# Kernel tuning notes

Hardware: AMD Instinct MI355X
Metric: run time of the kernel (lower is better)

## Reference

```python
import jax, jax.numpy as jnp
import numpy as np

BATCH, T, HID = 4, 2048, 1024
H = P = 1024  # input_dim and ssm_size (expand_ratio=1.0)
EPS = 1e-5
DISCRETIZATION = "IM"  # 'IM' or 'IMEX'


def setup_inputs() -> dict:
    key = jax.random.key(0)
    ks = jax.random.split(key, 10)
    std_b = 1.0 / np.sqrt(H)
    std_c = 1.0 / np.sqrt(P)
    u = lambda k, s, lo, hi: jax.random.uniform(k, s, jnp.float32, lo, hi)
    return {
        "hidden_states": jax.random.normal(ks[0], (BATCH, T, HID), jnp.float32),
        "Wi": jax.random.normal(ks[1], (H, HID), jnp.float32) / np.sqrt(HID),
        "Wg": jax.random.normal(ks[2], (H, HID), jnp.float32) / np.sqrt(HID),
        "Wo": jax.random.normal(ks[3], (HID, H), jnp.float32) / np.sqrt(H),
        "A_diag": u(ks[4], (P,), 0.0, 1.0),
        "B_param": u(ks[5], (P, H, 2), -std_b, std_b),
        "C_param": u(ks[6], (H, P, 2), -std_c, std_c),
        "D": jax.random.normal(ks[7], (H,), jnp.float32),
        "dt": u(ks[8], (P,), 0.0, 1.0),
        "norm_weight": jnp.ones((H,), jnp.float32),
    }


def _linoss(x, B_param, C_param, A_diag, dt_p, D):
    """LinOSS oscillatory SSM recurrence with complex B/C and diagonal A.
    x: (B,T,H) real input. State z,y in C^P (re/im stacked on last axis)."""
    A = jax.nn.relu(A_diag)       # (P,) nonneg frequencies
    dt = jax.nn.sigmoid(dt_p)     # (P,) timesteps in (0,1)
    # Bu_{re,im}[b,t,p] = sum_h x[b,t,h] * B_{re,im}[p,h]
    Bu = jnp.einsum('bth,phc->btpc', x, B_param)  # (B,T,P,2)
    if DISCRETIZATION == "IM":
        S = 1.0 / (1.0 + dt * dt * A)
        m11, m12, m21, m22 = S, -dt * A * S, dt * S, S
        f1, f2 = dt * S, dt * dt * S
    else:  # IMEX
        one = jnp.ones_like(dt)
        m11, m12, m21, m22 = one, -dt * A, dt, 1.0 - dt * dt * A
        f1, f2 = dt, dt * dt
    c = lambda v: v[None, :, None]  # broadcast (P,) -> (B,P,2)

    def step(carry, bu):
        z, y = carry  # each (B,P,2)
        z1 = c(m11) * z + c(m12) * y + c(f1) * bu
        y1 = c(m21) * z + c(m22) * y + c(f2) * bu
        return (z1, y1), y1

    z0 = jnp.zeros((x.shape[0], A.shape[0], 2), x.dtype)
    _, ys = jax.lax.scan(step, (z0, z0), jnp.swapaxes(Bu, 0, 1))
    ys = jnp.swapaxes(ys, 0, 1)  # (B,T,P,2)
    # o = Re(C @ y) + D * x
    o = (jnp.einsum('btp,hp->bth', ys[..., 0], C_param[..., 0])
         - jnp.einsum('btp,hp->bth', ys[..., 1], C_param[..., 1]))
    return o + x * D


def reference(hidden_states, Wi, Wg, Wo, A_diag, B_param, C_param, D, dt, norm_weight):
    x = hidden_states @ Wi.T                        # i_proj
    o = _linoss(x, B_param, C_param, A_diag, dt, D)  # fused_recurrent_linoss
    g = hidden_states @ Wg.T                        # g_proj
    # FusedRMSNormGated: rmsnorm(o) * weight * swish(g)
    o = o * jax.lax.rsqrt(jnp.mean(o * o, axis=-1, keepdims=True) + EPS) * norm_weight
    o = o * (g * jax.nn.sigmoid(g))
    return o @ Wo.T                                  # o_proj
```

## Files before the change

kernel.cpp:

```cpp
#include <hip/hip_runtime.h>
#include <hip/hip_bf16.h>
#include <math.h>

#define BB 4
#define TT 2048
#define HH 1024
#define PP 1024
#define MT 8192
#define C2 2048
#define NC 64
#define LCH 32

typedef __attribute__((ext_vector_type(8))) short  bf16x8;
typedef __attribute__((ext_vector_type(4))) float  f32x4;

__device__ __forceinline__ ushort f2bf(float f) {
    union { float f; unsigned u; } v; v.f = f;
    unsigned r = v.u + 0x7fffu + ((v.u >> 16) & 1u);
    return (ushort)(r >> 16);
}
__device__ __forceinline__ float bf2f(ushort h) {
    union { unsigned u; float f; } v; v.u = ((unsigned)h) << 16;
    return v.f;
}

__device__ __forceinline__ void gload16(const ushort* g, ushort* l) {
    __builtin_amdgcn_global_load_lds((const __attribute__((address_space(1))) void*)g,
                                     (__attribute__((address_space(3))) void*)l,
                                     16, 0, 0);
}
__device__ __forceinline__ void barrier_raw() { __builtin_amdgcn_s_barrier(); }
__device__ __forceinline__ void lgk0() { asm volatile("s_waitcnt lgkmcnt(0)" ::: "memory"); }
__device__ __forceinline__ void vm6()  { asm volatile("s_waitcnt vmcnt(6)"   ::: "memory"); }
__device__ __forceinline__ void vm0()  { asm volatile("s_waitcnt vmcnt(0)"   ::: "memory"); }

__global__ void convert_all(const float* __restrict__ hs, const float* __restrict__ Wi,
                            const float* __restrict__ Wg, const float* __restrict__ Wo,
                            ushort* __restrict__ hsb, ushort* __restrict__ Wigb,
                            ushort* __restrict__ Wob) {
    int i = blockIdx.x * 256 + threadIdx.x;
    const int HS4 = MT * HH / 4;
    const int W4  = HH * HH / 4;
    const float4* s;
    ushort4* d;
    if (i < HS4)               { s = (const float4*)hs + i;               d = (ushort4*)hsb  + i; }
    else if (i < HS4 + 2 * W4) { int j = i - HS4;
                                 s = (const float4*)(j < W4 ? Wi : Wg) + (j < W4 ? j : j - W4);
                                 d = (ushort4*)Wigb + j; }
    else                       { int j = i - HS4 - 2 * W4;
                                 s = (const float4*)Wo + j;               d = (ushort4*)Wob + j; }
    float4 v = *s;
    ushort4 o;
    o.x = f2bf(v.x); o.y = f2bf(v.y); o.z = f2bf(v.z); o.w = f2bf(v.w);
    *d = o;
}

__global__ void repack_B_bf(const float* __restrict__ src, ushort* __restrict__ dst) {
    int idx = blockIdx.x * 256 + threadIdx.x;
    int p = idx >> 10;
    int h = idx & 1023;
    float2 v = ((const float2*)src)[idx];
    dst[(size_t)p * HH + h]        = f2bf(v.x);
    dst[(size_t)(p + PP) * HH + h] = f2bf(v.y);
}

__global__ void repack_C_bf(const float* __restrict__ src, ushort* __restrict__ dst) {
    int idx = blockIdx.x * 256 + threadIdx.x;
    int h = idx >> 10;
    int p = idx & 1023;
    float2 v = ((const float2*)src)[idx];
    dst[(size_t)h * C2 + p]      = f2bf(v.x);
    dst[(size_t)h * C2 + PP + p] = f2bf(-v.y);
}

template<int BM, int STORE_BF16>
__global__ __launch_bounds__(512, 2) void gemm8p(
    const ushort* __restrict__ A, int lda,
    const ushort* __restrict__ B, int ldb,
    void* __restrict__ Cp, int ldc, int K, int nbx)
{
    constexpr int BN  = 256;
    constexpr int MR  = BM / 32;
    constexpr int MRH = MR / 2;
    constexpr int TA  = BM * 128;
    constexpr int TB  = BN * 128;
    __shared__ __align__(16) char smem[2 * TA + 2 * TB];

    const int bid = blockIdx.x;
    const int cpx = gridDim.x >> 3;
    const int wg  = (bid & 7) * cpx + (bid >> 3);
    const int by  = wg / nbx;
    const int bx  = wg - by * nbx;
    const int bm  = by * BM;
    const int bn  = bx * BN;

    const int tid  = threadIdx.x;
    const int wave = tid >> 6;
    const int lane = tid & 63;
    const int wr   = wave >> 2;
    const int wc   = wave & 3;
    const int lr   = lane & 15;
    const int kg   = lane >> 4;

    const int e  = (wave << 10) + ((lane << 4) ^ (((lane >> 3) & 7) << 4));
    const int r0 = e >> 7;
    const int c0 = (e & 127) >> 1;

    auto stA = [&](int bi, int u, int kt) {
        gload16(A + (size_t)(bm + u * 64 + r0) * lda + kt * 64 + c0,
                (ushort*)(smem + bi * TA + u * 8192 + (wave << 10)));
    };
    auto stB = [&](int bi, int u, int kt) {
        gload16(B + (size_t)(bn + u * 64 + r0) * ldb + kt * 64 + c0,
                (ushort*)(smem + 2 * TA + bi * TB + u * 8192 + (wave << 10)));
    };

    bf16x8 Af[MRH][2], Bf[4][2];
    auto ldsA = [&](int bi, int qm) {
#pragma unroll
        for (int f = 0; f < MRH; ++f)
#pragma unroll
            for (int kk = 0; kk < 2; ++kk) {
                int row = wr * (BM / 2) + qm * (BM / 4) + f * 16 + lr;
                int o = row * 128 + kk * 64 + kg * 16;
                o ^= (row & 7) << 4;
                Af[f][kk] = *(const bf16x8*)(smem + bi * TA + o);
            }
    };
    auto ldsB = [&](int bi) {
#pragma unroll
        for (int n = 0; n < 4; ++n)
#pragma unroll
            for (int kk = 0; kk < 2; ++kk) {
                int row = wc * 64 + n * 16 + lr;
                int o = row * 128 + kk * 64 + kg * 16;
                o ^= (row & 7) << 4;
                Bf[n][kk] = *(const bf16x8*)(smem + 2 * TA + bi * TB + o);
            }
    };

    f32x4 acc[MR][4];
#pragma unroll
    for (int m = 0; m < MR; ++m)
#pragma unroll
        for (int n = 0; n < 4; ++n)
#pragma unroll
            for (int i = 0; i < 4; ++i) acc[m][n][i] = 0.f;

    auto mfma16 = [&](int qm, int qn) {
        __builtin_amdgcn_s_setprio(1);
#pragma unroll
        for (int f = 0; f < MRH; ++f)
#pragma unroll
            for (int n2 = 0; n2 < 2; ++n2)
#pragma unroll
                for (int kk = 0; kk < 2; ++kk)
                    acc[qm * MRH + f][qn * 2 + n2] =
                        __builtin_amdgcn_mfma_f32_16x16x32_bf16(
                            Af[f][kk], Bf[qn * 2 + n2][kk],
                            acc[qm * MRH + f][qn * 2 + n2], 0, 0, 0);
        __builtin_amdgcn_s_setprio(0);
    };

    if constexpr (BM == 256) {
        stA(0, 0, 0); stA(0, 1, 0); stA(0, 2, 0); stA(0, 3, 0);
        stB(0, 0, 0); stB(0, 1, 0); stB(0, 2, 0); stB(0, 3, 0);
        stB(1, 0, 1); stB(1, 1, 1); stB(1, 2, 1); stB(1, 3, 1);
        stA(1, 0, 1); stA(1, 2, 1);
    } else {
        stA(0, 0, 0); stA(0, 1, 0);
        stB(0, 0, 0); stB(0, 1, 0); stB(0, 2, 0); stB(0, 3, 0);
        stA(1, 0, 1); stA(1, 1, 1);
        stB(1, 0, 1); stB(1, 1, 1); stB(1, 2, 1); stB(1, 3, 1);
    }
    vm6();
    barrier_raw();

    const int nIter = K >> 7;
    for (int J = 0; J < nIter; ++J) {
        const bool pf  = (J + 1 < nIter);
        const int  kt1 = 2 * J + 1, kt2 = 2 * J + 2, kt3 = 2 * J + 3;
        ldsA(0, 0); ldsB(0);
        if constexpr (BM == 256) { stA(1, 1, kt1); stA(1, 3, kt1); }
        barrier_raw(); lgk0(); mfma16(0, 0); barrier_raw();
        if (pf) { stB(0, 0, kt2); stB(0, 1, kt2); }
        barrier_raw(); lgk0(); mfma16(0, 1); barrier_raw();
        ldsA(0, 1);
        if (pf) { stB(0, 2, kt2); stB(0, 3, kt2); }
        barrier_raw(); lgk0(); mfma16(1, 0); barrier_raw();
        if (pf) {
            if constexpr (BM == 256) { stA(0, 0, kt2); stA(0, 2, kt2); }
            else                     { stA(0, 0, kt2); stA(0, 1, kt2); }
        }
        barrier_raw(); lgk0(); mfma16(1, 1);
        if (pf) vm6(); else vm0();
        barrier_raw();
        ldsA(1, 0); ldsB(1);
        if constexpr (BM == 256) { if (pf) { stA(0, 1, kt2); stA(0, 3, kt2); } }
        barrier_raw(); lgk0(); mfma16(0, 0); barrier_raw();
        if (pf) { stB(1, 0, kt3); stB(1, 1, kt3); }
        barrier_raw(); lgk0(); mfma16(0, 1); barrier_raw();
        ldsA(1, 1);
        if (pf) { stB(1, 2, kt3); stB(1, 3, kt3); }
        barrier_raw(); lgk0(); mfma16(1, 0); barrier_raw();
        if (pf) {
            if constexpr (BM == 256) { stA(1, 0, kt3); stA(1, 2, kt3); }
            else                     { stA(1, 0, kt3); stA(1, 1, kt3); }
        }
        barrier_raw(); lgk0(); mfma16(1, 1);
        if (pf) vm6(); else vm0();
        barrier_raw();
    }

#pragma unroll
    for (int mf = 0; mf < MR; ++mf) {
#pragma unroll
        for (int n = 0; n < 4; ++n) {
            int col = bn + wc * 64 + n * 16 + lr;
#pragma unroll
            for (int i = 0; i < 4; ++i) {
                int row = bm + wr * (BM / 2) + mf * 16 + kg * 4 + i;
                float v = acc[mf][n][i];
                if (STORE_BF16)
                    ((ushort*)Cp)[(size_t)row * ldc + col] = f2bf(v);
                else
                    ((float*)Cp)[(size_t)row * ldc + col]  = v;
            }
        }
    }
}

__device__ __forceinline__ void linoss_coeffs(const float* A_diag, const float* dt_p,
                                              int p, float& m11, float& m12,
                                              float& m21, float& m22,
                                              float& f1, float& f2) {
    float A  = fmaxf(A_diag[p], 0.f);
    float dt = 1.f / (1.f + expf(-dt_p[p]));
    float S  = 1.f / (1.f + dt * dt * A);
    m11 = S;        m12 = -dt * A * S;
    m21 = dt * S;   m22 = S;
    f1  = dt * S;   f2  = dt * dt * S;
}

__global__ void scan_passA(const ushort* __restrict__ Bu,
                           const float* __restrict__ A_diag,
                           const float* __restrict__ dt_p,
                           float2* __restrict__ sEnd) {
    int c = blockIdx.x * 256 + threadIdx.x;
    int b = blockIdx.y;
    int j = blockIdx.z;
    float m11, m12, m21, m22, f1, f2;
    linoss_coeffs(A_diag, dt_p, c & 1023, m11, m12, m21, m22, f1, f2);
    const ushort* bu = Bu + ((size_t)(b * TT + j * LCH)) * C2 + c;
    float z = 0.f, y = 0.f;
#pragma unroll 8
    for (int i = 0; i < LCH; ++i) {
        float u  = bf2f(bu[(size_t)i * C2]);
        float z1 = m11 * z + m12 * y + f1 * u;
        float y1 = m21 * z + m22 * y + f2 * u;
        z = z1; y = y1;
    }
    sEnd[((size_t)j * BB + b) * C2 + c] = make_float2(z, y);
}

__global__ void scan_combine(const float* __restrict__ A_diag,
                             const float* __restrict__ dt_p,
                             const float2* __restrict__ sEnd,
                             float2* __restrict__ sInit) {
    int idx = blockIdx.x * 256 + threadIdx.x;
    int c = idx & (C2 - 1);
    int b = idx >> 11;
    float m11, m12, m21, m22, f1, f2;
    linoss_coeffs(A_diag, dt_p, c & 1023, m11, m12, m21, m22, f1, f2);
    float e11 = m11, e12 = m12, e21 = m21, e22 = m22;
#pragma unroll
    for (int s = 0; s < 5; ++s) {
        float n11 = e11 * e11 + e12 * e21;
        float n12 = e11 * e12 + e12 * e22;
        float n21 = e21 * e11 + e22 * e21;
        float n22 = e21 * e12 + e22 * e22;
        e11 = n11; e12 = n12; e21 = n21; e22 = n22;
    }
    float z = 0.f, y = 0.f;
    for (int j = 0; j < NC; ++j) {
        size_t off = ((size_t)j * BB + b) * C2 + c;
        sInit[off] = make_float2(z, y);
        float2 le = sEnd[off];
        float z1 = e11 * z + e12 * y + le.x;
        float y1 = e21 * z + e22 * y + le.y;
        z = z1; y = y1;
    }
}

__global__ void scan_passB(const ushort* __restrict__ Bu,
                           const float* __restrict__ A_diag,
                           const float* __restrict__ dt_p,
                           const float2* __restrict__ sInit,
                           ushort* __restrict__ YSb) {
    int c = blockIdx.x * 256 + threadIdx.x;
    int b = blockIdx.y;
    int j = blockIdx.z;
    float m11, m12, m21, m22, f1, f2;
    linoss_coeffs(A_diag, dt_p, c & 1023, m11, m12, m21, m22, f1, f2);
    float2 s0 = sInit[((size_t)j * BB + b) * C2 + c];
    float z = s0.x, y = s0.y;
    const ushort* bu = Bu  + ((size_t)(b * TT + j * LCH)) * C2 + c;
    ushort*       ys = YSb + ((size_t)(b * TT + j * LCH)) * C2 + c;
#pragma unroll 8
    for (int i = 0; i < LCH; ++i) {
        float u  = bf2f(bu[(size_t)i * C2]);
        float z1 = m11 * z + m12 * y + f1 * u;
        float y1 = m21 * z + m22 * y + f2 * u;
        z = z1; y = y1;
        ys[(size_t)i * C2] = f2bf(y);
    }
}

__global__ void rmsgate_kernel(const float* __restrict__ O,
                               const ushort* __restrict__ XGb,
                               const float* __restrict__ Dv,
                               const float* __restrict__ nw,
                               ushort* __restrict__ V) {
    int m = blockIdx.x;
    int t = threadIdx.x;
    float4  o4 = ((const float4*)(O + (size_t)m * HH))[t];
    ushort4 x4 = ((const ushort4*)(XGb + (size_t)m * C2))[t];
    float4  d4 = ((const float4*)Dv)[t];
    float of[4];
    of[0] = o4.x + d4.x * bf2f(x4.x);
    of[1] = o4.y + d4.y * bf2f(x4.y);
    of[2] = o4.z + d4.z * bf2f(x4.z);
    of[3] = o4.w + d4.w * bf2f(x4.w);
    float ss = of[0]*of[0] + of[1]*of[1] + of[2]*of[2] + of[3]*of[3];
#pragma unroll
    for (int o = 32; o > 0; o >>= 1) ss += __shfl_down(ss, o);
    __shared__ float wsum[4];
    if ((t & 63) == 0) wsum[t >> 6] = ss;
    __syncthreads();
    float tot = wsum[0] + wsum[1] + wsum[2] + wsum[3];
    float r = rsqrtf(tot * (1.f / (float)HH) + 1e-5f);

    ushort4 g4 = ((const ushort4*)(XGb + (size_t)m * C2 + HH))[t];
    float4  w4 = ((const float4*)nw)[t];
    float g[4] = {bf2f(g4.x), bf2f(g4.y), bf2f(g4.z), bf2f(g4.w)};
    float w[4] = {w4.x, w4.y, w4.z, w4.w};
    ushort4 vout;
    ushort* vo = &vout.x;
#pragma unroll
    for (int i = 0; i < 4; ++i) {
        float sw = g[i] / (1.f + expf(-g[i]));
        vo[i] = f2bf(of[i] * r * w[i] * sw);
    }
    ((ushort4*)(V + (size_t)m * HH))[t] = vout;
}

extern "C" void kernel_launch(void* const* d_in, const int* in_sizes, int n_in,
                              void* d_out, int out_size, void* d_ws, size_t ws_size,
                              hipStream_t stream) {
    const float* hs      = (const float*)d_in[0];
    const float* Wi      = (const float*)d_in[1];
    const float* Wg      = (const float*)d_in[2];
    const float* Wo      = (const float*)d_in[3];
    const float* A_diag  = (const float*)d_in[4];
    const float* B_param = (const float*)d_in[5];
    const float* C_param = (const float*)d_in[6];
    const float* Dv      = (const float*)d_in[7];
    const float* dtp     = (const float*)d_in[8];
    const float* nw      = (const float*)d_in[9];
    float* out = (float*)d_out;

    char* ws = (char*)d_ws;
    ushort* hsb  = (ushort*)ws;                                   ws += (size_t)MT * HH * 2;
    ushort* Wigb = (ushort*)ws;                                   ws += (size_t)C2 * HH * 2;
    ushort* Wob  = (ushort*)ws;                                   ws += (size_t)HH * HH * 2;
    ushort* Bpkb = (ushort*)ws;                                   ws += (size_t)C2 * HH * 2;
    ushort* Cpkb = (ushort*)ws;                                   ws += (size_t)HH * C2 * 2;
    ushort* XGb  = (ushort*)ws;                                   ws += (size_t)MT * C2 * 2;
    ushort* Bu   = (ushort*)ws;                                   ws += (size_t)MT * C2 * 2;
    ushort* YSb  = (ushort*)ws;                                   ws += (size_t)MT * C2 * 2;
    float*  O    = (float*)ws;                                    ws += (size_t)MT * HH * 4;
    ushort* Vb   = (ushort*)ws;                                   ws += (size_t)MT * HH * 2;
    float2* sEnd  = (float2*)ws;                                  ws += (size_t)NC * BB * C2 * 8;
    float2* sInit = (float2*)ws;

    dim3 blk(256);

    convert_all<<<dim3((MT * HH / 4 + 3 * HH * HH / 4) / 256), blk, 0, stream>>>(
        hs, Wi, Wg, Wo, hsb, Wigb, Wob);
    repack_B_bf<<<dim3((PP * HH) / 256), blk, 0, stream>>>(B_param, Bpkb);
    repack_C_bf<<<dim3((HH * PP) / 256), blk, 0, stream>>>(C_param, Cpkb);

    gemm8p<256, 1><<<dim3(256), dim3(512), 0, stream>>>(
        hsb, HH, Wigb, HH, XGb, C2, HH, 8);

    gemm8p<256, 1><<<dim3(256), dim3(512), 0, stream>>>(
        XGb, C2, Bpkb, HH, Bu, C2, HH, 8);

    scan_passA<<<dim3(C2 / 256, BB, NC), blk, 0, stream>>>(Bu, A_diag, dtp, sEnd);
    scan_combine<<<dim3((BB * C2) / 256), blk, 0, stream>>>(A_diag, dtp, sEnd, sInit);
    scan_passB<<<dim3(C2 / 256, BB, NC), blk, 0, stream>>>(Bu, A_diag, dtp, sInit, YSb);

    gemm8p<128, 0><<<dim3(256), dim3(512), 0, stream>>>(
        YSb, C2, Cpkb, C2, O, HH, C2, 4);

    rmsgate_kernel<<<dim3(MT), blk, 0, stream>>>(O, XGb, Dv, nw, Vb);

    gemm8p<128, 0><<<dim3(256), dim3(512), 0, stream>>>(
        Vb, HH, Wob, HH, out, HH, HH, 4);
}
```

Baseline: 196.5 us.

## Use triple-buffered 128x256 GEMM, merge prep kernels, store SSM output as bf16

The GEMM is rewritten from a double-buffered two-k-tile pipeline into a triple-buffered single k-tile loop with a fixed 128x256 tile. The i/g and Bu GEMMs now launch 512 blocks instead of 256. The three conversion and repack kernels are merged into one launch. The C-projection output O is stored as bf16 instead of fp32, halving its write and read traffic, at some precision cost before the RMS norm. LDS use rises to 3*(TA+TB), about 144KB, which may limit occupancy to one block per CU.

Measured after the change: 204.3 us. 1.04x slower.

```diff
diff --git a/kernel.cpp b/kernel.cpp
--- a/kernel.cpp
+++ b/kernel.cpp
@@ -34,57 +34,59 @@
 __device__ __forceinline__ void vm6()  { asm volatile("s_waitcnt vmcnt(6)"   ::: "memory"); }
 __device__ __forceinline__ void vm0()  { asm volatile("s_waitcnt vmcnt(0)"   ::: "memory"); }
 
-__global__ void convert_all(const float* __restrict__ hs, const float* __restrict__ Wi,
-                            const float* __restrict__ Wg, const float* __restrict__ Wo,
-                            ushort* __restrict__ hsb, ushort* __restrict__ Wigb,
-                            ushort* __restrict__ Wob) {
+#define HS4   (MT * HH / 4)
+#define W4    (HH * HH / 4)
+#define PREP_CONV  (HS4 + 3 * W4)
+#define PREP_B     (PREP_CONV + PP * HH)
+#define PREP_TOT   (PREP_B + HH * PP)
+
+__global__ void prep_all(const float* __restrict__ hs, const float* __restrict__ Wi,
+                         const float* __restrict__ Wg, const float* __restrict__ Wo,
+                         const float* __restrict__ B_param, const float* __restrict__ C_param,
+                         ushort* __restrict__ hsb, ushort* __restrict__ Wigb,
+                         ushort* __restrict__ Wob, ushort* __restrict__ Bpkb,
+                         ushort* __restrict__ Cpkb) {
     int i = blockIdx.x * 256 + threadIdx.x;
-    const int HS4 = MT * HH / 4;
-    const int W4  = HH * HH / 4;
-    const float4* s;
-    ushort4* d;
-    if (i < HS4)               { s = (const float4*)hs + i;               d = (ushort4*)hsb  + i; }
-    else if (i < HS4 + 2 * W4) { int j = i - HS4;
-                                 s = (const float4*)(j < W4 ? Wi : Wg) + (j < W4 ? j : j - W4);
-                                 d = (ushort4*)Wigb + j; }
-    else                       { int j = i - HS4 - 2 * W4;
-                                 s = (const float4*)Wo + j;               d = (ushort4*)Wob + j; }
-    float4 v = *s;
-    ushort4 o;
-    o.x = f2bf(v.x); o.y = f2bf(v.y); o.z = f2bf(v.z); o.w = f2bf(v.w);
-    *d = o;
-}
-
-__global__ void repack_B_bf(const float* __restrict__ src, ushort* __restrict__ dst) {
-    int idx = blockIdx.x * 256 + threadIdx.x;
-    int p = idx >> 10;
-    int h = idx & 1023;
-    float2 v = ((const float2*)src)[idx];
-    dst[(size_t)p * HH + h]        = f2bf(v.x);
-    dst[(size_t)(p + PP) * HH + h] = f2bf(v.y);
-}
-
-__global__ void repack_C_bf(const float* __restrict__ src, ushort* __restrict__ dst) {
-    int idx = blockIdx.x * 256 + threadIdx.x;
-    int h = idx >> 10;
-    int p = idx & 1023;
-    float2 v = ((const float2*)src)[idx];
-    dst[(size_t)h * C2 + p]      = f2bf(v.x);
-    dst[(size_t)h * C2 + PP + p] = f2bf(-v.y);
-}
-
-template<int BM, int STORE_BF16>
-__global__ __launch_bounds__(512, 2) void gemm8p(
+    if (i < PREP_CONV) {
+        const float4* s;
+        ushort4* d;
+        if (i < HS4)              { s = (const float4*)hs + i;  d = (ushort4*)hsb + i; }
+        else if (i < HS4 + 2*W4)  { int j = i - HS4;
+                                    s = (const float4*)(j < W4 ? Wi : Wg) + (j < W4 ? j : j - W4);
+                                    d = (ushort4*)Wigb + j; }
+        else                      { int j = i - HS4 - 2*W4;
+                                    s = (const float4*)Wo + j; d = (ushort4*)Wob + j; }
+        float4 v = *s;
+        ushort4 o;
+        o.x = f2bf(v.x); o.y = f2bf(v.y); o.z = f2bf(v.z); o.w = f2bf(v.w);
+        *d = o;
+    } else if (i < PREP_B) {
+        int idx = i - PREP_CONV;
+        int p = idx >> 10;
+        int h = idx & 1023;
+        float2 v = ((const float2*)B_param)[idx];
+        Bpkb[(size_t)p * HH + h]        = f2bf(v.x);
+        Bpkb[(size_t)(p + PP) * HH + h] = f2bf(v.y);
+    } else {
+        int idx = i - PREP_B;
+        int h = idx >> 10;
+        int p = idx & 1023;
+        float2 v = ((const float2*)C_param)[idx];
+        Cpkb[(size_t)h * C2 + p]      = f2bf(v.x);
+        Cpkb[(size_t)h * C2 + PP + p] = f2bf(-v.y);
+    }
+}
+
+template<int STORE_BF16>
+__global__ __launch_bounds__(512, 2) void gemm3b(
     const ushort* __restrict__ A, int lda,
     const ushort* __restrict__ B, int ldb,
     void* __restrict__ Cp, int ldc, int K, int nbx)
 {
-    constexpr int BN  = 256;
-    constexpr int MR  = BM / 32;
-    constexpr int MRH = MR / 2;
-    constexpr int TA  = BM * 128;
-    constexpr int TB  = BN * 128;
-    __shared__ __align__(16) char smem[2 * TA + 2 * TB];
+    constexpr int BM = 128, BN = 256;
+    constexpr int TA = BM * 128;
+    constexpr int TB = BN * 128;
+    __shared__ __align__(16) char smem[3 * (TA + TB)];
 
     const int bid = blockIdx.x;
     const int cpx = gridDim.x >> 3;
@@ -112,16 +114,16 @@
     };
     auto stB = [&](int bi, int u, int kt) {
         gload16(B + (size_t)(bn + u * 64 + r0) * ldb + kt * 64 + c0,
-                (ushort*)(smem + 2 * TA + bi * TB + u * 8192 + (wave << 10)));
-    };
-
-    bf16x8 Af[MRH][2], Bf[4][2];
+                (ushort*)(smem + 3 * TA + bi * TB + u * 8192 + (wave << 10)));
+    };
+
+    bf16x8 Af[2][2], Bf[4][2];
     auto ldsA = [&](int bi, int qm) {
 #pragma unroll
-        for (int f = 0; f < MRH; ++f)
+        for (int f = 0; f < 2; ++f)
 #pragma unroll
             for (int kk = 0; kk < 2; ++kk) {
-                int row = wr * (BM / 2) + qm * (BM / 4) + f * 16 + lr;
+                int row = wr * 64 + qm * 32 + f * 16 + lr;
                 int o = row * 128 + kk * 64 + kg * 16;
                 o ^= (row & 7) << 4;
                 Af[f][kk] = *(const bf16x8*)(smem + bi * TA + o);
@@ -135,91 +137,68 @@
                 int row = wc * 64 + n * 16 + lr;
                 int o = row * 128 + kk * 64 + kg * 16;
                 o ^= (row & 7) << 4;
-                Bf[n][kk] = *(const bf16x8*)(smem + 2 * TA + bi * TB + o);
+                Bf[n][kk] = *(const bf16x8*)(smem + 3 * TA + bi * TB + o);
             }
     };
 
-    f32x4 acc[MR][4];
-#pragma unroll
-    for (int m = 0; m < MR; ++m)
+    f32x4 acc[4][4];
+#pragma unroll
+    for (int m = 0; m < 4; ++m)
 #pragma unroll
         for (int n = 0; n < 4; ++n)
 #pragma unroll
             for (int i = 0; i < 4; ++i) acc[m][n][i] = 0.f;
 
-    auto mfma16 = [&](int qm, int qn) {
+    auto cl = [&](int qm) {
         __builtin_amdgcn_s_setprio(1);
 #pragma unroll
-        for (int f = 0; f < MRH; ++f)
-#pragma unroll
-            for (int n2 = 0; n2 < 2; ++n2)
+        for (int f = 0; f < 2; ++f)
+#pragma unroll
+            for (int n = 0; n < 4; ++n)
 #pragma unroll
                 for (int kk = 0; kk < 2; ++kk)
-                    acc[qm * MRH + f][qn * 2 + n2] =
+                    acc[qm * 2 + f][n] =
                         __builtin_amdgcn_mfma_f32_16x16x32_bf16(
-                            Af[f][kk], Bf[qn * 2 + n2][kk],
-                            acc[qm * MRH + f][qn * 2 + n2], 0, 0, 0);
+                            Af[f][kk], Bf[n][kk], acc[qm * 2 + f][n], 0, 0, 0);
         __builtin_amdgcn_s_setprio(0);
     };
 
-    if constexpr (BM == 256) {
-        stA(0, 0, 0); stA(0, 1, 0); stA(0, 2, 0); stA(0, 3, 0);
-        stB(0, 0, 0); stB(0, 1, 0); stB(0, 2, 0); stB(0, 3, 0);
-        stB(1, 0, 1); stB(1, 1, 1); stB(1, 2, 1); stB(1, 3, 1);
-        stA(1, 0, 1); stA(1, 2, 1);
-    } else {
-        stA(0, 0, 0); stA(0, 1, 0);
-        stB(0, 0, 0); stB(0, 1, 0); stB(0, 2, 0); stB(0, 3, 0);
-        stA(1, 0, 1); stA(1, 1, 1);
-        stB(1, 0, 1); stB(1, 1, 1); stB(1, 2, 1); stB(1, 3, 1);
-    }
+    stB(0, 0, 0); stB(0, 1, 0); stB(0, 2, 0); stB(0, 3, 0);
+    stA(0, 0, 0); stA(0, 1, 0);
+    stB(1, 0, 1); stB(1, 1, 1); stB(1, 2, 1); stB(1, 3, 1);
+    stA(1, 0, 1); stA(1, 1, 1);
     vm6();
     barrier_raw();
 
-    const int nIter = K >> 7;
-    for (int J = 0; J < nIter; ++J) {
-        const bool pf  = (J + 1 < nIter);
-        const int  kt1 = 2 * J + 1, kt2 = 2 * J + 2, kt3 = 2 * J + 3;
-        ldsA(0, 0); ldsB(0);
-        if constexpr (BM == 256) { stA(1, 1, kt1); stA(1, 3, kt1); }
-        barrier_raw(); lgk0(); mfma16(0, 0); barrier_raw();
-        if (pf) { stB(0, 0, kt2); stB(0, 1, kt2); }
-        barrier_raw(); lgk0(); mfma16(0, 1); barrier_raw();
-        ldsA(0, 1);
-        if (pf) { stB(0, 2, kt2); stB(0, 3, kt2); }
-        barrier_raw(); lgk0(); mfma16(1, 0); barrier_raw();
-        if (pf) {
-            if constexpr (BM == 256) { stA(0, 0, kt2); stA(0, 2, kt2); }
-            else                     { stA(0, 0, kt2); stA(0, 1, kt2); }
-        }
-        barrier_raw(); lgk0(); mfma16(1, 1);
+    const int nT = K >> 6;
+    int bt = 0, b1 = 1, b2 = 2;
+    for (int t = 0; t < nT; ++t) {
+        const bool pf = (t + 2 < nT);
+        ldsA(bt, 0); ldsB(bt);
+        if (pf) { stB(b2, 0, t + 2); stB(b2, 1, t + 2);
+                  stB(b2, 2, t + 2); stB(b2, 3, t + 2); }
+        barrier_raw();
+        cl(0);
+        lgk0();
+        barrier_raw();
+        ldsA(bt, 1);
+        if (pf) { stA(b2, 0, t + 2); stA(b2, 1, t + 2); }
+        barrier_raw();
+        cl(1);
+        lgk0();
         if (pf) vm6(); else vm0();
         barrier_raw();
-        ldsA(1, 0); ldsB(1);
-        if constexpr (BM == 256) { if (pf) { stA(0, 1, kt2); stA(0, 3, kt2); } }
-        barrier_raw(); lgk0(); mfma16(0, 0); barrier_raw();
-        if (pf) { stB(1, 0, kt3); stB(1, 1, kt3); }
-        barrier_raw(); lgk0(); mfma16(0, 1); barrier_raw();
-        ldsA(1, 1);
-        if (pf) { stB(1, 2, kt3); stB(1, 3, kt3); }
-        barrier_raw(); lgk0(); mfma16(1, 0); barrier_raw();
-        if (pf) {
-            if constexpr (BM == 256) { stA(1, 0, kt3); stA(1, 2, kt3); }
-            else                     { stA(1, 0, kt3); stA(1, 1, kt3); }
-        }
-        barrier_raw(); lgk0(); mfma16(1, 1);
-        if (pf) vm6(); else vm0();
-        barrier_raw();
-    }
-
-#pragma unroll
-    for (int mf = 0; mf < MR; ++mf) {
+        int tmp = bt; bt = b1; b1 = b2; b2 = tmp;
+    }
+
+#pragma unroll
+    for (int mf = 0; mf < 4; ++mf) {
 #pragma unroll
         for (int n = 0; n < 4; ++n) {
             int col = bn + wc * 64 + n * 16 + lr;
 #pragma unroll
             for (int i = 0; i < 4; ++i) {
-                int row = bm + wr * (BM / 2) + mf * 16 + kg * 4 + i;
+                int row = bm + wr * 64 + mf * 16 + kg * 4 + i;
                 float v = acc[mf][n][i];
                 if (STORE_BF16)
                     ((ushort*)Cp)[(size_t)row * ldc + col] = f2bf(v);
@@ -316,21 +295,21 @@
     }
 }
 
-__global__ void rmsgate_kernel(const float* __restrict__ O,
+__global__ void rmsgate_kernel(const ushort* __restrict__ O,
                                const ushort* __restrict__ XGb,
                                const float* __restrict__ Dv,
                                const float* __restrict__ nw,
                                ushort* __restrict__ V) {
     int m = blockIdx.x;
     int t = threadIdx.x;
-    float4  o4 = ((const float4*)(O + (size_t)m * HH))[t];
+    ushort4 o4 = ((const ushort4*)(O + (size_t)m * HH))[t];
     ushort4 x4 = ((const ushort4*)(XGb + (size_t)m * C2))[t];
     float4  d4 = ((const float4*)Dv)[t];
     float of[4];
-    of[0] = o4.x + d4.x * bf2f(x4.x);
-    of[1] = o4.y + d4.y * bf2f(x4.y);
-    of[2] = o4.z + d4.z * bf2f(x4.z);
-    of[3] = o4.w + d4.w * bf2f(x4.w);
+    of[0] = bf2f(o4.x) + d4.x * bf2f(x4.x);
+    of[1] = bf2f(o4.y) + d4.y * bf2f(x4.y);
+    of[2] = bf2f(o4.z) + d4.z * bf2f(x4.z);
+    of[3] = bf2f(o4.w) + d4.w * bf2f(x4.w);
     float ss = of[0]*of[0] + of[1]*of[1] + of[2]*of[2] + of[3]*of[3];
 #pragma unroll
     for (int o = 32; o > 0; o >>= 1) ss += __shfl_down(ss, o);
@@ -378,33 +357,31 @@
     ushort* XGb  = (ushort*)ws;                                   ws += (size_t)MT * C2 * 2;
     ushort* Bu   = (ushort*)ws;                                   ws += (size_t)MT * C2 * 2;
     ushort* YSb  = (ushort*)ws;                                   ws += (size_t)MT * C2 * 2;
-    float*  O    = (float*)ws;                                    ws += (size_t)MT * HH * 4;
+    ushort* O    = (ushort*)ws;                                   ws += (size_t)MT * HH * 2;
     ushort* Vb   = (ushort*)ws;                                   ws += (size_t)MT * HH * 2;
     float2* sEnd  = (float2*)ws;                                  ws += (size_t)NC * BB * C2 * 8;
     float2* sInit = (float2*)ws;
 
     dim3 blk(256);
 
-    convert_all<<<dim3((MT * HH / 4 + 3 * HH * HH / 4) / 256), blk, 0, stream>>>(
-        hs, Wi, Wg, Wo, hsb, Wigb, Wob);
-    repack_B_bf<<<dim3((PP * HH) / 256), blk, 0, stream>>>(B_param, Bpkb);
-    repack_C_bf<<<dim3((HH * PP) / 256), blk, 0, stream>>>(C_param, Cpkb);
-
-    gemm8p<256, 1><<<dim3(256), dim3(512), 0, stream>>>(
+    prep_all<<<dim3(PREP_TOT / 256), blk, 0, stream>>>(
+        hs, Wi, Wg, Wo, B_param, C_param, hsb, Wigb, Wob, Bpkb, Cpkb);
+
+    gemm3b<1><<<dim3(512), dim3(512), 0, stream>>>(
         hsb, HH, Wigb, HH, XGb, C2, HH, 8);
 
-    gemm8p<256, 1><<<dim3(256), dim3(512), 0, stream>>>(
+    gemm3b<1><<<dim3(512), dim3(512), 0, stream>>>(
         XGb, C2, Bpkb, HH, Bu, C2, HH, 8);
 
     scan_passA<<<dim3(C2 / 256, BB, NC), blk, 0, stream>>>(Bu, A_diag, dtp, sEnd);
     scan_combine<<<dim3((BB * C2) / 256), blk, 0, stream>>>(A_diag, dtp, sEnd, sInit);
     scan_passB<<<dim3(C2 / 256, BB, NC), blk, 0, stream>>>(Bu, A_diag, dtp, sInit, YSb);
 
-    gemm8p<128, 0><<<dim3(256), dim3(512), 0, stream>>>(
+    gemm3b<1><<<dim3(256), dim3(512), 0, stream>>>(
         YSb, C2, Cpkb, C2, O, HH, C2, 4);
 
     rmsgate_kernel<<<dim3(MT), blk, 0, stream>>>(O, XGb, Dv, nw, Vb);
 
-    gemm8p<128, 0><<<dim3(256), dim3(512), 0, stream>>>(
+    gemm3b<0><<<dim3(256), dim3(512), 0, stream>>>(
         Vb, HH, Wob, HH, out, HH, HH, 4);
 }
```
